# Kernel optimization log

Measured on AMD Instinct MI355X. Metric: run time of the kernel, lower is better.

## Reference

```python
import jax, jax.numpy as jnp
import numpy as np

SEQ, BATCH, IN_CH = 4096, 8, 256
HID = 256
LOOKBACK, LOOKAHEAD = 1, 0
K = LOOKBACK + 1 + LOOKAHEAD  # conv kernel size = 2


def setup_inputs() -> dict:
    key = jax.random.key(0)
    k1, k2, k3, k4, k5, k6 = jax.random.split(key, 6)
    X = jax.random.normal(k1, (SEQ, BATCH, IN_CH), dtype=jnp.float32)
    hidden = jax.random.normal(k2, (BATCH, HID), dtype=jnp.float32)
    scale = 1.0 / np.sqrt(IN_CH * K)
    Wz = jax.random.normal(k3, (HID, IN_CH, K), dtype=jnp.float32) * scale
    bz = jax.random.normal(k4, (HID,), dtype=jnp.float32) * scale
    Wf = jax.random.normal(k5, (HID, IN_CH, K), dtype=jnp.float32) * scale
    bf = jax.random.normal(k6, (HID,), dtype=jnp.float32) * scale
    return {"X": X, "hidden": hidden, "Wz": Wz, "bz": bz, "Wf": Wf, "bf": bf}


def _conv1d(Xp, W, b):
    # Xp: (B, C_in, S_pad); W: (C_out, C_in, K) -> (B, C_out, S)
    y = jax.lax.conv_general_dilated(
        Xp, W, window_strides=(1,), padding='VALID',
        dimension_numbers=('NCW', 'OIW', 'NCW'))
    return y + b[None, :, None]


def reference(X, hidden, Wz, bz, Wf, bf):
    # pad seq dim: lookback zeros in front, lookahead behind
    X_pad = jnp.pad(X, ((LOOKBACK, LOOKAHEAD), (0, 0), (0, 0)))
    Xp = jnp.transpose(X_pad, (1, 2, 0))  # (B, C_in, S_pad)

    Z = jnp.transpose(_conv1d(Xp, Wz, bz), (2, 0, 1))  # (S, B, H)
    F = jnp.transpose(_conv1d(Xp, Wf, bf), (2, 0, 1))  # (S, B, H)

    Z = Z * jax.nn.sigmoid(1.702 * Z)  # QuickGELU
    F = jax.nn.sigmoid(F)

    def step(h, fz):
        f, z = fz
        h = f * z + (1.0 - f) * h
        return h, h

    h_last, H = jax.lax.scan(step, hidden, (F, Z))
    return H, h_last[None]  # (S,B,H), (1,B,H)
```

## Files before the change

### kernel.cpp

```cpp
#include <hip/hip_runtime.h>


#define SEQn 4096
#define NCH 2048
#define CHUNK 32
#define NCHUNK 128

typedef __attribute__((ext_vector_type(8))) short bf16x8;
typedef __attribute__((ext_vector_type(4))) float floatx4;

__device__ __forceinline__ unsigned short f2bf(float x) {
  unsigned int u = __float_as_uint(x);
  u += 0x7fffu + ((u >> 16) & 1u);
  return (unsigned short)(u >> 16);
}
__device__ __forceinline__ float bf2f(ushort u) {
  return __uint_as_float((unsigned int)u << 16);
}
__device__ __forceinline__ float sigf(float x) {
  return __builtin_amdgcn_rcpf(1.0f + __expf(-x));
}

__global__ void pack_kernel(const float* __restrict__ X,
                            const float* __restrict__ Wz, const float* __restrict__ Wf,
                            ushort* __restrict__ Xbf, ushort* __restrict__ Bm) {
  if (blockIdx.x < 1024) {
    int idx = blockIdx.x * 256 + threadIdx.x;
    int n = idx >> 9, kin = idx & 511;
    const float* W = (n < 256) ? Wz : Wf;
    int h = n & 255, c = kin & 255, tap = kin >> 8;
    Bm[idx] = f2bf(W[h * 512 + c * 2 + tap]);
  } else {
    int idx = (blockIdx.x - 1024) * 256 + threadIdx.x;
    const int total4 = ((SEQn + 1) * NCH) / 4;
    if (idx >= total4) return;
    const int pad4 = NCH / 4;
    float4 v;
    if (idx < pad4) { v.x = 0.f; v.y = 0.f; v.z = 0.f; v.w = 0.f; }
    else v = ((const float4*)X)[idx - pad4];
    ushort4 o;
    o.x = f2bf(v.x); o.y = f2bf(v.y); o.z = f2bf(v.z); o.w = f2bf(v.w);
    ((ushort4*)Xbf)[idx] = o;
  }
}

__global__ __launch_bounds__(256) void gemm_kernel(
    const ushort* __restrict__ Xbf, const ushort* __restrict__ Bm,
    const float* __restrict__ bz, const float* __restrict__ bfb,
    ushort* __restrict__ zout, ushort* __restrict__ fout) {
  __shared__ __align__(16) char smem_raw[24576];
  ushort* sA = (ushort*)smem_raw;
  ushort* sB = sA + 4096;
  ushort* sT = (ushort*)smem_raw;

  const int tid  = threadIdx.x;
  const int wave = tid >> 6;
  const int lane = tid & 63;
  const int quad = lane >> 4;
  const int lrow = lane & 15;
  const int wm = wave >> 1;
  const int wn = wave & 1;
  const int bm = blockIdx.x;
  const int bn = blockIdx.y;

  floatx4 acc[2][4];
#pragma unroll
  for (int i = 0; i < 2; ++i)
#pragma unroll
    for (int j = 0; j < 4; ++j)
      acc[i][j] = (floatx4){0.f, 0.f, 0.f, 0.f};

  int rowA[2], gkoA[2], rowB[4], gkoB[4];
#pragma unroll
  for (int it = 0; it < 2; ++it) {
    int g = it * 256 + wave * 64 + lane;
    int row = g >> 3, s = g & 7;
    rowA[it] = row;
    gkoA[it] = (s ^ (row & 7)) * 8;
  }
#pragma unroll
  for (int it = 0; it < 4; ++it) {
    int g = it * 256 + wave * 64 + lane;
    int row = g >> 3, s = g & 7;
    rowB[it] = row;
    gkoB[it] = (s ^ (row & 7)) * 8;
  }
  char* ldsA = smem_raw + wave * 1024 + (lane << 4);
  char* ldsB = smem_raw + 8192 + wave * 1024 + (lane << 4);

  const ushort* Arow = Xbf + (size_t)(bm * 64) * 256;
  const ushort* Brow = Bm + (size_t)(bn * 128) * 512;

  for (int k0 = 0; k0 < 512; k0 += 64) {
    __syncthreads();
#pragma unroll
    for (int it = 0; it < 2; ++it) {
      const int kk = k0 + gkoA[it];
      const int cA = (kk < 256) ? kk : kk + 1792;
      __builtin_amdgcn_global_load_lds(
          (const __attribute__((address_space(1))) void*)(Arow + (size_t)rowA[it] * 256 + cA),
          (__attribute__((address_space(3))) void*)(ldsA + it * 4096), 16, 0, 0);
    }
#pragma unroll
    for (int it = 0; it < 4; ++it) {
      const int kk = k0 + gkoB[it];
      __builtin_amdgcn_global_load_lds(
          (const __attribute__((address_space(1))) void*)(Brow + (size_t)rowB[it] * 512 + kk),
          (__attribute__((address_space(3))) void*)(ldsB + it * 4096), 16, 0, 0);
    }
    __syncthreads();

    bf16x8 af[2][2], bfr[4][2];
#pragma unroll
    for (int fi = 0; fi < 2; ++fi) {
      const int r = wm * 32 + fi * 16 + lrow;
#pragma unroll
      for (int ks = 0; ks < 2; ++ks) {
        const int s = (ks * 4 + quad) ^ (r & 7);
        af[fi][ks] = *(const bf16x8*)&sA[r * 64 + s * 8];
      }
    }
#pragma unroll
    for (int fj = 0; fj < 4; ++fj) {
      const int r = wn * 64 + fj * 16 + lrow;
#pragma unroll
      for (int ks = 0; ks < 2; ++ks) {
        const int s = (ks * 4 + quad) ^ (r & 7);
        bfr[fj][ks] = *(const bf16x8*)&sB[r * 64 + s * 8];
      }
    }
#pragma unroll
    for (int ks = 0; ks < 2; ++ks)
#pragma unroll
      for (int fi = 0; fi < 2; ++fi)
#pragma unroll
        for (int fj = 0; fj < 4; ++fj)
          acc[fi][fj] = __builtin_amdgcn_mfma_f32_16x16x32_bf16(af[fi][ks], bfr[fj][ks], acc[fi][fj], 0, 0, 0);
  }

  const bool isZ = (bn < 2);
  ushort* gout = isZ ? zout : fout;
  const int ncol0 = (bn & 1) * 128;
  const float* bias = isZ ? bz : bfb;
  float bv[4];
#pragma unroll
  for (int fj = 0; fj < 4; ++fj)
    bv[fj] = bias[ncol0 + wn * 64 + fj * 16 + lrow];

  __syncthreads();
#pragma unroll
  for (int fi = 0; fi < 2; ++fi)
#pragma unroll
    for (int fj = 0; fj < 4; ++fj)
#pragma unroll
      for (int r = 0; r < 4; ++r) {
        float v = acc[fi][fj][r] + bv[fj];
        float o = isZ ? (v * sigf(1.702f * v)) : sigf(v);
        sT[(wm * 32 + fi * 16 + quad * 4 + r) * 136 + wn * 64 + fj * 16 + lrow] = f2bf(o);
      }
  __syncthreads();
#pragma unroll
  for (int it = 0; it < 4; ++it) {
    int e = tid + it * 256;
    int row = e >> 4, seg = e & 15;
    uint4 v = *(uint4*)&sT[row * 136 + seg * 8];
    *(uint4*)(gout + (size_t)(bm * 64 + row) * 256 + ncol0 + seg * 8) = v;
  }
}

__global__ void scanA_kernel(const ushort* __restrict__ z, const ushort* __restrict__ f,
                             float* __restrict__ Ac, float* __restrict__ Cc) {
  int t = blockIdx.x * blockDim.x + threadIdx.x;
  int ch2 = t & 1023;
  int j = t >> 10;
  const size_t base = (size_t)j * CHUNK * NCH + 2 * ch2;
  const ushort* zp = z + base;
  const ushort* fp = f + base;
  float A0 = 1.0f, C0 = 0.0f, A1 = 1.0f, C1 = 0.0f;
#pragma unroll
  for (int i = 0; i < CHUNK; ++i) {
    ushort2 fv = *(const ushort2*)(fp + (size_t)i * NCH);
    ushort2 zv = *(const ushort2*)(zp + (size_t)i * NCH);
    float f0 = bf2f(fv.x), f1 = bf2f(fv.y);
    float a0 = 1.0f - f0, a1 = 1.0f - f1;
    C0 = fmaf(a0, C0, f0 * bf2f(zv.x)); A0 *= a0;
    C1 = fmaf(a1, C1, f1 * bf2f(zv.y)); A1 *= a1;
  }
  float2 Av = {A0, A1}, Cv = {C0, C1};
  *(float2*)(Ac + (size_t)j * NCH + 2 * ch2) = Av;
  *(float2*)(Cc + (size_t)j * NCH + 2 * ch2) = Cv;
}

__global__ void scanB_kernel(const float* __restrict__ hidden,
                             const float* __restrict__ Ac, const float* __restrict__ Cc,
                             float* __restrict__ Hs) {
  const int lane = threadIdx.x & 63;
  const int ch = blockIdx.x * 4 + (threadIdx.x >> 6);
  const int j0 = 2 * lane, j1 = 2 * lane + 1;
  float a0 = Ac[j0 * NCH + ch], c0 = Cc[j0 * NCH + ch];
  float a1 = Ac[j1 * NCH + ch], c1 = Cc[j1 * NCH + ch];
  float a = a0 * a1;
  float c = fmaf(a1, c0, c1);
#pragma unroll
  for (int d = 1; d < 64; d <<= 1) {
    float pa = __shfl_up(a, d, 64);
    float pc = __shfl_up(c, d, 64);
    if (lane >= d) { c = fmaf(a, pc, c); a *= pa; }
  }
  float xa = __shfl_up(a, 1, 64), xc = __shfl_up(c, 1, 64);
  if (lane == 0) { xa = 1.0f; xc = 0.0f; }
  float h0 = hidden[ch];
  float hs0 = fmaf(xa, h0, xc);
  Hs[j0 * NCH + ch] = hs0;
  Hs[j1 * NCH + ch] = fmaf(a0, hs0, c0);
}

__global__ void scanC_kernel(const ushort* __restrict__ z, const ushort* __restrict__ f,
                             const float* __restrict__ Hs, float* __restrict__ out) {
  int t = blockIdx.x * blockDim.x + threadIdx.x;
  int ch2 = t & 1023;
  int j = t >> 10;
  float2 hv = *(const float2*)(Hs + (size_t)j * NCH + 2 * ch2);
  float h0 = hv.x, h1 = hv.y;
  const size_t base = (size_t)j * CHUNK * NCH + 2 * ch2;
  const ushort* zp = z + base;
  const ushort* fp = f + base;
  float* op = out + base;
#pragma unroll
  for (int i = 0; i < CHUNK; ++i) {
    ushort2 fv = *(const ushort2*)(fp + (size_t)i * NCH);
    ushort2 zv = *(const ushort2*)(zp + (size_t)i * NCH);
    float f0 = bf2f(fv.x), f1 = bf2f(fv.y);
    h0 = fmaf(f0, bf2f(zv.x) - h0, h0);
    h1 = fmaf(f1, bf2f(zv.y) - h1, h1);
    float2 o = {h0, h1};
    *(float2*)(op + (size_t)i * NCH) = o;
  }
  if (j == NCHUNK - 1) {
    float2 o = {h0, h1};
    *(float2*)(out + (size_t)SEQn * NCH + 2 * ch2) = o;
  }
}

extern "C" void kernel_launch(void* const* d_in, const int* in_sizes, int n_in,
                              void* d_out, int out_size, void* d_ws, size_t ws_size,
                              hipStream_t stream) {
  const float* X      = (const float*)d_in[0];
  const float* hidden = (const float*)d_in[1];
  const float* Wz     = (const float*)d_in[2];
  const float* bz     = (const float*)d_in[3];
  const float* Wf     = (const float*)d_in[4];
  const float* bfb    = (const float*)d_in[5];
  float* out = (float*)d_out;

  char* ws = (char*)d_ws;
  ushort* zbf = (ushort*)ws;
  ushort* fbf = (ushort*)(ws + 16777216);
  ushort* Xbf = (ushort*)(ws + 33554432);
  ushort* Bm  = (ushort*)(ws + 50335744);
  float* Ac = (float*)(ws + 33554432);
  float* Cc = (float*)(ws + 34603008);
  float* Hs = (float*)(ws + 35651584);

  pack_kernel<<<9218, 256, 0, stream>>>(X, Wz, Wf, Xbf, Bm);
  dim3 ggrid(512, 4);
  gemm_kernel<<<ggrid, 256, 0, stream>>>(Xbf, Bm, bz, bfb, zbf, fbf);
  scanA_kernel<<<512, 256, 0, stream>>>(zbf, fbf, Ac, Cc);
  scanB_kernel<<<512, 256, 0, stream>>>(hidden, Ac, Cc, Hs);
  scanC_kernel<<<512, 256, 0, stream>>>(zbf, fbf, Hs, out);
}
```

Measured before the change: 139.5 us.

## Fuse chunk-local scan into GEMM epilogue with paired Z/F tiles per block

Each GEMM block now computes matching Z and F column tiles (64 columns each) for the same 64 rows, which is 8 timesteps across 8 batches. The epilogue then computes the chunk's (A, C) scan coefficients directly from LDS and writes them out, so the separate scanA pass that reread z/f from global memory is gone. The chunk size drops from 32 to 8, which gives 512 chunks. scanB now does a serial 8-element prefix per lane before the wave scan, and scanC launches 4x more threads. The cost is more work in the GEMM epilogue and larger Ac/Cc/Hs buffers, which are moved to a new workspace offset.

```diff
diff --git a/kernel.cpp b/kernel.cpp
--- a/kernel.cpp
+++ b/kernel.cpp
@@ -3,8 +3,8 @@
 
 #define SEQn 4096
 #define NCH 2048
-#define CHUNK 32
-#define NCHUNK 128
+#define CHUNK 8
+#define NCHUNK 512
 
 typedef __attribute__((ext_vector_type(8))) short bf16x8;
 typedef __attribute__((ext_vector_type(4))) float floatx4;
@@ -47,11 +47,11 @@
 __global__ __launch_bounds__(256) void gemm_kernel(
     const ushort* __restrict__ Xbf, const ushort* __restrict__ Bm,
     const float* __restrict__ bz, const float* __restrict__ bfb,
-    ushort* __restrict__ zout, ushort* __restrict__ fout) {
+    ushort* __restrict__ zout, ushort* __restrict__ fout,
+    float* __restrict__ Ac, float* __restrict__ Cc) {
   __shared__ __align__(16) char smem_raw[24576];
   ushort* sA = (ushort*)smem_raw;
   ushort* sB = sA + 4096;
-  ushort* sT = (ushort*)smem_raw;
 
   const int tid  = threadIdx.x;
   const int wave = tid >> 6;
@@ -62,15 +62,18 @@
   const int wn = wave & 1;
   const int bm = blockIdx.x;
   const int bn = blockIdx.y;
-
-  floatx4 acc[2][4];
-#pragma unroll
-  for (int i = 0; i < 2; ++i)
-#pragma unroll
-    for (int j = 0; j < 4; ++j)
-      acc[i][j] = (floatx4){0.f, 0.f, 0.f, 0.f};
-
-  int rowA[2], gkoA[2], rowB[4], gkoB[4];
+  const int ncol0 = bn * 64;
+
+  floatx4 acc[2][2][2];
+#pragma unroll
+  for (int zf = 0; zf < 2; ++zf)
+#pragma unroll
+    for (int i = 0; i < 2; ++i)
+#pragma unroll
+      for (int j = 0; j < 2; ++j)
+        acc[zf][i][j] = (floatx4){0.f, 0.f, 0.f, 0.f};
+
+  int rowA[2], gkoA[2], rowBG[4], gkoB[4];
 #pragma unroll
   for (int it = 0; it < 2; ++it) {
     int g = it * 256 + wave * 64 + lane;
@@ -82,14 +85,13 @@
   for (int it = 0; it < 4; ++it) {
     int g = it * 256 + wave * 64 + lane;
     int row = g >> 3, s = g & 7;
-    rowB[it] = row;
+    rowBG[it] = (row < 64) ? (ncol0 + row) : (192 + ncol0 + row);
     gkoB[it] = (s ^ (row & 7)) * 8;
   }
   char* ldsA = smem_raw + wave * 1024 + (lane << 4);
   char* ldsB = smem_raw + 8192 + wave * 1024 + (lane << 4);
 
   const ushort* Arow = Xbf + (size_t)(bm * 64) * 256;
-  const ushort* Brow = Bm + (size_t)(bn * 128) * 512;
 
   for (int k0 = 0; k0 < 512; k0 += 64) {
     __syncthreads();
@@ -105,12 +107,12 @@
     for (int it = 0; it < 4; ++it) {
       const int kk = k0 + gkoB[it];
       __builtin_amdgcn_global_load_lds(
-          (const __attribute__((address_space(1))) void*)(Brow + (size_t)rowB[it] * 512 + kk),
+          (const __attribute__((address_space(1))) void*)(Bm + (size_t)rowBG[it] * 512 + kk),
           (__attribute__((address_space(3))) void*)(ldsB + it * 4096), 16, 0, 0);
     }
     __syncthreads();
 
-    bf16x8 af[2][2], bfr[4][2];
+    bf16x8 af[2][2];
 #pragma unroll
     for (int fi = 0; fi < 2; ++fi) {
       const int r = wm * 32 + fi * 16 + lrow;
@@ -121,74 +123,78 @@
       }
     }
 #pragma unroll
-    for (int fj = 0; fj < 4; ++fj) {
-      const int r = wn * 64 + fj * 16 + lrow;
-#pragma unroll
-      for (int ks = 0; ks < 2; ++ks) {
-        const int s = (ks * 4 + quad) ^ (r & 7);
-        bfr[fj][ks] = *(const bf16x8*)&sB[r * 64 + s * 8];
+    for (int zf = 0; zf < 2; ++zf) {
+      bf16x8 bfr[2][2];
+#pragma unroll
+      for (int fj = 0; fj < 2; ++fj) {
+        const int r = zf * 64 + wn * 32 + fj * 16 + lrow;
+#pragma unroll
+        for (int ks = 0; ks < 2; ++ks) {
+          const int s = (ks * 4 + quad) ^ (r & 7);
+          bfr[fj][ks] = *(const bf16x8*)&sB[r * 64 + s * 8];
+        }
       }
-    }
-#pragma unroll
-    for (int ks = 0; ks < 2; ++ks)
-#pragma unroll
-      for (int fi = 0; fi < 2; ++fi)
-#pragma unroll
-        for (int fj = 0; fj < 4; ++fj)
-          acc[fi][fj] = __builtin_amdgcn_mfma_f32_16x16x32_bf16(af[fi][ks], bfr[fj][ks], acc[fi][fj], 0, 0, 0);
-  }
-
-  const bool isZ = (bn < 2);
-  ushort* gout = isZ ? zout : fout;
-  const int ncol0 = (bn & 1) * 128;
-  const float* bias = isZ ? bz : bfb;
-  float bv[4];
-#pragma unroll
-  for (int fj = 0; fj < 4; ++fj)
-    bv[fj] = bias[ncol0 + wn * 64 + fj * 16 + lrow];
+#pragma unroll
+      for (int ks = 0; ks < 2; ++ks)
+#pragma unroll
+        for (int fi = 0; fi < 2; ++fi)
+#pragma unroll
+          for (int fj = 0; fj < 2; ++fj)
+            acc[zf][fi][fj] = __builtin_amdgcn_mfma_f32_16x16x32_bf16(af[fi][ks], bfr[fj][ks], acc[zf][fi][fj], 0, 0, 0);
+    }
+  }
+
+  float bvz[2], bvf[2];
+#pragma unroll
+  for (int fj = 0; fj < 2; ++fj) {
+    bvz[fj] = bz[ncol0 + wn * 32 + fj * 16 + lrow];
+    bvf[fj] = bfb[ncol0 + wn * 32 + fj * 16 + lrow];
+  }
 
   __syncthreads();
+  ushort* sTz = (ushort*)smem_raw;
+  ushort* sTf = sTz + 64 * 72;
 #pragma unroll
   for (int fi = 0; fi < 2; ++fi)
 #pragma unroll
-    for (int fj = 0; fj < 4; ++fj)
+    for (int fj = 0; fj < 2; ++fj)
 #pragma unroll
       for (int r = 0; r < 4; ++r) {
-        float v = acc[fi][fj][r] + bv[fj];
-        float o = isZ ? (v * sigf(1.702f * v)) : sigf(v);
-        sT[(wm * 32 + fi * 16 + quad * 4 + r) * 136 + wn * 64 + fj * 16 + lrow] = f2bf(o);
+        int row = wm * 32 + fi * 16 + quad * 4 + r;
+        int col = wn * 32 + fj * 16 + lrow;
+        float vz = acc[0][fi][fj][r] + bvz[fj];
+        float vf = acc[1][fi][fj][r] + bvf[fj];
+        sTz[row * 72 + col] = f2bf(vz * sigf(1.702f * vz));
+        sTf[row * 72 + col] = f2bf(sigf(vf));
       }
   __syncthreads();
-#pragma unroll
-  for (int it = 0; it < 4; ++it) {
+
+#pragma unroll
+  for (int half = 0; half < 2; ++half) {
+    int cl = tid + half * 256;
+    int b = cl >> 6, h = cl & 63;
+    float A = 1.f, C = 0.f;
+#pragma unroll
+    for (int i = 0; i < 8; ++i) {
+      float zv = bf2f(sTz[(i * 8 + b) * 72 + h]);
+      float fv = bf2f(sTf[(i * 8 + b) * 72 + h]);
+      float a = 1.f - fv;
+      C = fmaf(a, C, fv * zv); A *= a;
+    }
+    size_t o = (size_t)bm * NCH + b * 256 + ncol0 + h;
+    Ac[o] = A; Cc[o] = C;
+  }
+
+#pragma unroll
+  for (int it = 0; it < 2; ++it) {
     int e = tid + it * 256;
-    int row = e >> 4, seg = e & 15;
-    uint4 v = *(uint4*)&sT[row * 136 + seg * 8];
-    *(uint4*)(gout + (size_t)(bm * 64 + row) * 256 + ncol0 + seg * 8) = v;
-  }
-}
-
-__global__ void scanA_kernel(const ushort* __restrict__ z, const ushort* __restrict__ f,
-                             float* __restrict__ Ac, float* __restrict__ Cc) {
-  int t = blockIdx.x * blockDim.x + threadIdx.x;
-  int ch2 = t & 1023;
-  int j = t >> 10;
-  const size_t base = (size_t)j * CHUNK * NCH + 2 * ch2;
-  const ushort* zp = z + base;
-  const ushort* fp = f + base;
-  float A0 = 1.0f, C0 = 0.0f, A1 = 1.0f, C1 = 0.0f;
-#pragma unroll
-  for (int i = 0; i < CHUNK; ++i) {
-    ushort2 fv = *(const ushort2*)(fp + (size_t)i * NCH);
-    ushort2 zv = *(const ushort2*)(zp + (size_t)i * NCH);
-    float f0 = bf2f(fv.x), f1 = bf2f(fv.y);
-    float a0 = 1.0f - f0, a1 = 1.0f - f1;
-    C0 = fmaf(a0, C0, f0 * bf2f(zv.x)); A0 *= a0;
-    C1 = fmaf(a1, C1, f1 * bf2f(zv.y)); A1 *= a1;
-  }
-  float2 Av = {A0, A1}, Cv = {C0, C1};
-  *(float2*)(Ac + (size_t)j * NCH + 2 * ch2) = Av;
-  *(float2*)(Cc + (size_t)j * NCH + 2 * ch2) = Cv;
+    int row = e >> 3, s8 = e & 7;
+    uint4 vz = *(uint4*)&sTz[row * 72 + s8 * 8];
+    uint4 vf = *(uint4*)&sTf[row * 72 + s8 * 8];
+    size_t o = (size_t)(bm * 64 + row) * 256 + ncol0 + s8 * 8;
+    *(uint4*)(zout + o) = vz;
+    *(uint4*)(fout + o) = vf;
+  }
 }
 
 __global__ void scanB_kernel(const float* __restrict__ hidden,
@@ -196,11 +202,17 @@
                              float* __restrict__ Hs) {
   const int lane = threadIdx.x & 63;
   const int ch = blockIdx.x * 4 + (threadIdx.x >> 6);
-  const int j0 = 2 * lane, j1 = 2 * lane + 1;
-  float a0 = Ac[j0 * NCH + ch], c0 = Cc[j0 * NCH + ch];
-  float a1 = Ac[j1 * NCH + ch], c1 = Cc[j1 * NCH + ch];
-  float a = a0 * a1;
-  float c = fmaf(a1, c0, c1);
+  float av[8], cv[8];
+  float a = 1.f, c = 0.f;
+#pragma unroll
+  for (int i = 0; i < 8; ++i) {
+    av[i] = a; cv[i] = c;
+    int j = lane * 8 + i;
+    float Aj = Ac[(size_t)j * NCH + ch];
+    float Cj = Cc[(size_t)j * NCH + ch];
+    c = fmaf(Aj, c, Cj);
+    a *= Aj;
+  }
 #pragma unroll
   for (int d = 1; d < 64; d <<= 1) {
     float pa = __shfl_up(a, d, 64);
@@ -208,11 +220,12 @@
     if (lane >= d) { c = fmaf(a, pc, c); a *= pa; }
   }
   float xa = __shfl_up(a, 1, 64), xc = __shfl_up(c, 1, 64);
-  if (lane == 0) { xa = 1.0f; xc = 0.0f; }
+  if (lane == 0) { xa = 1.f; xc = 0.f; }
   float h0 = hidden[ch];
-  float hs0 = fmaf(xa, h0, xc);
-  Hs[j0 * NCH + ch] = hs0;
-  Hs[j1 * NCH + ch] = fmaf(a0, hs0, c0);
+  float hs = fmaf(xa, h0, xc);
+#pragma unroll
+  for (int i = 0; i < 8; ++i)
+    Hs[(size_t)(lane * 8 + i) * NCH + ch] = fmaf(av[i], hs, cv[i]);
 }
 
 __global__ void scanC_kernel(const ushort* __restrict__ z, const ushort* __restrict__ f,
@@ -258,14 +271,13 @@
   ushort* fbf = (ushort*)(ws + 16777216);
   ushort* Xbf = (ushort*)(ws + 33554432);
   ushort* Bm  = (ushort*)(ws + 50335744);
-  float* Ac = (float*)(ws + 33554432);
-  float* Cc = (float*)(ws + 34603008);
-  float* Hs = (float*)(ws + 35651584);
+  float* Ac = (float*)(ws + 52428800);
+  float* Cc = (float*)(ws + 56623104);
+  float* Hs = (float*)(ws + 60817408);
 
   pack_kernel<<<9218, 256, 0, stream>>>(X, Wz, Wf, Xbf, Bm);
   dim3 ggrid(512, 4);
-  gemm_kernel<<<ggrid, 256, 0, stream>>>(Xbf, Bm, bz, bfb, zbf, fbf);
-  scanA_kernel<<<512, 256, 0, stream>>>(zbf, fbf, Ac, Cc);
+  gemm_kernel<<<ggrid, 256, 0, stream>>>(Xbf, Bm, bz, bfb, zbf, fbf, Ac, Cc);
   scanB_kernel<<<512, 256, 0, stream>>>(hidden, Ac, Cc, Hs);
-  scanC_kernel<<<512, 256, 0, stream>>>(zbf, fbf, Hs, out);
-}
+  scanC_kernel<<<2048, 256, 0, stream>>>(zbf, fbf, Hs, out);
+}
```

After: 147.9 us. 6.0% more time.
